# Kernel optimization log

Measured on AMD Instinct MI355X. Metric: run time of the kernel, lower is better.

Reference implementation:

```python
import jax, jax.numpy as jnp
import numpy as np

B, CTX, DRAFT, D = 2, 4096, 512, 2048
H, KVH, HD = 16, 4, 128
N_REP = H // KVH
EPS = 1e-6
THETA = 10000.0
SCALE = 1.0 / np.sqrt(HD).astype(np.float32)


def setup_inputs() -> dict:
    key = jax.random.key(0)
    ks = jax.random.split(key, 6)
    return {
        "draft_hidden": jax.random.normal(ks[0], (B, DRAFT, D), jnp.float32),
        "context_hidden": jax.random.normal(ks[1], (B, CTX, D), jnp.float32),
        "Wq": jax.random.normal(ks[2], (H * HD, D), jnp.float32) * 0.02,
        "Wk": jax.random.normal(ks[3], (KVH * HD, D), jnp.float32) * 0.02,
        "Wv": jax.random.normal(ks[4], (KVH * HD, D), jnp.float32) * 0.02,
        "Wo": jax.random.normal(ks[5], (D, H * HD), jnp.float32) * 0.02,
        "q_norm_w": jnp.ones((HD,), jnp.float32),
        "k_norm_w": jnp.ones((HD,), jnp.float32),
        "context_position_ids": jnp.broadcast_to(jnp.arange(CTX, dtype=jnp.int32), (B, CTX)),
        "draft_position_ids": jnp.broadcast_to(CTX + jnp.arange(DRAFT, dtype=jnp.int32), (B, DRAFT)),
    }


def _rms_norm(x, w):
    # per-head RMSNorm over last dim (head_dim), computed in fp32
    v = jnp.mean(jnp.square(x.astype(jnp.float32)), axis=-1, keepdims=True)
    return (w * (x.astype(jnp.float32) * jax.lax.rsqrt(v + EPS))).astype(x.dtype)


def _rotate_half(x):
    x1, x2 = jnp.split(x, 2, axis=-1)
    return jnp.concatenate((-x2, x1), axis=-1)


def _rope(x, pos):
    # x: [B, nH, S, HD], pos: [B, S] int -> cos/sin gathered per position
    inv_freq = 1.0 / (THETA ** (jnp.arange(0, HD, 2, dtype=jnp.float32) / HD))  # [HD/2]
    freqs = pos.astype(jnp.float32)[:, None, :, None] * inv_freq  # [B,1,S,HD/2]
    emb = jnp.concatenate((freqs, freqs), axis=-1)  # [B,1,S,HD]
    return x * jnp.cos(emb) + _rotate_half(x) * jnp.sin(emb)


def reference(draft_hidden, context_hidden, Wq, Wk, Wv, Wo, q_norm_w, k_norm_w,
              context_position_ids, draft_position_ids):
    bsz, draft_len, _ = draft_hidden.shape
    ctx_len = context_hidden.shape[1]
    total_len = ctx_len + draft_len

    # Q from draft hidden only
    q = (draft_hidden @ Wq.T).reshape(bsz, draft_len, H, HD)
    q = _rms_norm(q, q_norm_w).transpose(0, 2, 1, 3)  # [B,H,Sq,HD]

    # Dual-source KV: context then draft, shared projections
    kv_in = jnp.concatenate([context_hidden, draft_hidden], axis=1)  # [B,total,D]
    k = (kv_in @ Wk.T).reshape(bsz, total_len, KVH, HD)
    v = (kv_in @ Wv.T).reshape(bsz, total_len, KVH, HD).transpose(0, 2, 1, 3)
    k = _rms_norm(k, k_norm_w).transpose(0, 2, 1, 3)  # [B,KVH,total,HD]

    full_position_ids = jnp.concatenate([context_position_ids, draft_position_ids], axis=1)
    q = _rope(q, draft_position_ids)
    k = _rope(k, full_position_ids)

    # GQA expansion (repeat each kv head n_rep times contiguously)
    k = jnp.repeat(k, N_REP, axis=1)  # [B,H,total,HD]
    v = jnp.repeat(v, N_REP, axis=1)

    # full (unmasked) scaled dot-product attention, block_mask=None path
    scores = jnp.einsum('bhqd,bhkd->bhqk', q, k) * SCALE
    probs = jax.nn.softmax(scores, axis=-1)
    attn = jnp.einsum('bhqk,bhkd->bhqd', probs, v)  # [B,H,Sq,HD]

    attn = attn.transpose(0, 2, 1, 3).reshape(bsz, draft_len, H * HD)
    return attn @ Wo.T
```

## Files before the change

### kernel.cpp

```cpp
#include <hip/hip_runtime.h>
#include <stdint.h>

#define B_ 2
#define CTX_ 4096
#define DRAFT_ 512
#define D_ 2048
#define H_ 16
#define KVH_ 4
#define HD_ 128
#define TOT_ 4608
#define NSPLIT 4
#define SPLIT_LEN (TOT_ / NSPLIT)

using bf16x8 = __attribute__((ext_vector_type(8))) short;
using f32x4  = __attribute__((ext_vector_type(4))) float;
using f32x16 = __attribute__((ext_vector_type(16))) float;

__device__ __forceinline__ unsigned short f2bf(float x) {
  unsigned int u = __float_as_uint(x);
  u += 0x7fffu + ((u >> 16) & 1u);
  return (unsigned short)(u >> 16);
}

__device__ __forceinline__ unsigned cvtpk(float lo, float hi) {
  unsigned r;
  asm("v_cvt_pk_bf16_f32 %0, %1, %2" : "=v"(r) : "v"(lo), "v"(hi));
  return r;
}

__device__ __forceinline__ void gload16(const void* g, void* l) {
  __builtin_amdgcn_global_load_lds((const __attribute__((address_space(1))) void*)g,
                                   (__attribute__((address_space(3))) void*)l, 16, 0, 0);
}

__device__ __forceinline__ f32x16 vbroad16(float x) {
  f32x16 v;
#pragma unroll
  for (int i = 0; i < 16; ++i) v[i] = x;
  return v;
}

__global__ __launch_bounds__(256, 4)
void conv_kernel(const float* __restrict__ ctx, const float* __restrict__ draft,
                 const float* __restrict__ wq, const float* __restrict__ wk,
                 const float* __restrict__ wv, const float* __restrict__ wo,
                 unsigned short* __restrict__ kv, unsigned short* __restrict__ wqb,
                 unsigned short* __restrict__ wkb, unsigned short* __restrict__ wvb,
                 unsigned short* __restrict__ wob) {
  long t = (long)blockIdx.x * 256 + threadIdx.x;
  const long NKV = (long)B_ * TOT_ * D_ / 8;
  const long NWQ = 2048L * 2048 / 8;
  const long NWK = 512L * 2048 / 8;
  const float* src;
  unsigned short* dst;
  if (t < NKV) {
    long i = t * 8;
    int b = (int)(i / ((long)TOT_ * D_));
    long rem = i - (long)b * TOT_ * D_;
    int r = (int)(rem / D_);
    int c = (int)(rem - (long)r * D_);
    if (r < CTX_) src = ctx + ((long)(b * CTX_ + r)) * D_ + c;
    else          src = draft + ((long)(b * DRAFT_ + (r - CTX_))) * D_ + c;
    dst = kv + i;
  } else if (t < NKV + NWQ) {
    long l = t - NKV; src = wq + l * 8; dst = wqb + l * 8;
  } else if (t < NKV + NWQ + NWK) {
    long l = t - NKV - NWQ; src = wk + l * 8; dst = wkb + l * 8;
  } else if (t < NKV + NWQ + 2 * NWK) {
    long l = t - NKV - NWQ - NWK; src = wv + l * 8; dst = wvb + l * 8;
  } else {
    long l = t - NKV - NWQ - 2 * NWK; src = wo + l * 8; dst = wob + l * 8;
  }
  float4 a = ((const float4*)src)[0];
  float4 b4 = ((const float4*)src)[1];
  uint4 o;
  o.x = (unsigned)f2bf(a.x) | ((unsigned)f2bf(a.y) << 16);
  o.y = (unsigned)f2bf(a.z) | ((unsigned)f2bf(a.w) << 16);
  o.z = (unsigned)f2bf(b4.x) | ((unsigned)f2bf(b4.y) << 16);
  o.w = (unsigned)f2bf(b4.z) | ((unsigned)f2bf(b4.w) << 16);
  *((uint4*)dst) = o;
}

template <int BM, int BN>
__device__ __forceinline__ void gemm_body(const unsigned short* __restrict__ A,
                                          const unsigned short* __restrict__ W,
                                          float* __restrict__ C, int ld, int kLen,
                                          int N, unsigned short* lds) {
  constexpr int MT = BM / 32;
  constexpr int NT = BN / 32;
  constexpr int BUF = (BM + BN) * 64;
  constexpr int LOADS = BM / 32 + BN / 32;
  const int tid = threadIdx.x;
  const int lane = tid & 63, wid = tid >> 6;
  const int g = lane >> 4, r16 = lane & 15;
  const int wm = wid >> 1, wn = wid & 1;

  f32x4 zero = {0.f, 0.f, 0.f, 0.f};
  f32x4 acc[MT][NT];
#pragma unroll
  for (int i = 0; i < MT; ++i)
#pragma unroll
    for (int j = 0; j < NT; ++j) acc[i][j] = zero;

  auto stage = [&](int kb, unsigned short* buf) {
    unsigned short* As = buf;
    unsigned short* Bs = buf + BM * 64;
#pragma unroll
    for (int is = 0; is < BM / 32; ++is) {
      int row = is * 32 + (tid >> 3);
      int sl = (tid & 7) ^ (row & 7);
      gload16(A + (long)row * ld + kb + sl * 8, As + is * 2048 + wid * 512);
    }
#pragma unroll
    for (int is = 0; is < BN / 32; ++is) {
      int row = is * 32 + (tid >> 3);
      int sl = (tid & 7) ^ (row & 7);
      gload16(W + (long)row * ld + kb + sl * 8, Bs + is * 2048 + wid * 512);
    }
  };

  stage(0, lds);
  const int nk = kLen >> 6;
  for (int t = 0; t < nk; ++t) {
    if (t + 1 < nk) {
      stage((t + 1) << 6, lds + ((t + 1) & 1) * BUF);
      if constexpr (LOADS == 8)      asm volatile("s_waitcnt vmcnt(8)" ::: "memory");
      else if constexpr (LOADS == 6) asm volatile("s_waitcnt vmcnt(6)" ::: "memory");
      else if constexpr (LOADS == 4) asm volatile("s_waitcnt vmcnt(4)" ::: "memory");
      else                           asm volatile("s_waitcnt vmcnt(0)" ::: "memory");
    } else {
      asm volatile("s_waitcnt vmcnt(0)" ::: "memory");
    }
    __builtin_amdgcn_s_barrier();
    __builtin_amdgcn_sched_barrier(0);
    unsigned short* As = lds + (t & 1) * BUF;
    unsigned short* Bs = As + BM * 64;
#pragma unroll
    for (int kh = 0; kh < 2; ++kh) {
      bf16x8 af[MT], bfr[NT];
#pragma unroll
      for (int i = 0; i < MT; ++i) {
        int row = wm * (BM / 2) + i * 16 + r16;
        int sl = (kh * 4 + g) ^ (row & 7);
        af[i] = *(const bf16x8*)(As + row * 64 + sl * 8);
      }
#pragma unroll
      for (int j = 0; j < NT; ++j) {
        int row = wn * (BN / 2) + j * 16 + r16;
        int sl = (kh * 4 + g) ^ (row & 7);
        bfr[j] = *(const bf16x8*)(Bs + row * 64 + sl * 8);
      }
#pragma unroll
      for (int i = 0; i < MT; ++i)
#pragma unroll
        for (int j = 0; j < NT; ++j)
          acc[i][j] = __builtin_amdgcn_mfma_f32_16x16x32_bf16(af[i], bfr[j], acc[i][j], 0, 0, 0);
    }
    __builtin_amdgcn_sched_barrier(0);
    __builtin_amdgcn_s_barrier();
  }
#pragma unroll
  for (int i = 0; i < MT; ++i)
#pragma unroll
    for (int j = 0; j < NT; ++j)
#pragma unroll
      for (int e = 0; e < 4; ++e) {
        int row = wm * (BM / 2) + i * 16 + g * 4 + e;
        int col = wn * (BN / 2) + j * 16 + r16;
        C[(long)row * N + col] = acc[i][j][e];
      }
}

__global__ __launch_bounds__(256, 2)
void qkv_kernel(const unsigned short* __restrict__ kvb,
                const unsigned short* __restrict__ wqb,
                const unsigned short* __restrict__ wkvb, float* __restrict__ qraw,
                float* __restrict__ kvraw) {
  __shared__ unsigned short lds[2 * 256 * 64];
  int id = (blockIdx.x & 7) * 88 + (blockIdx.x >> 3);
  if (id < 128) {
    int b = id >> 6, mb = (id >> 4) & 3, nb = id & 15;
    const unsigned short* A = kvb + ((long)b * TOT_ + CTX_ + mb * 128) * 2048;
    const unsigned short* W = wqb + (long)nb * 128 * 2048;
    float* C = qraw + ((long)b * 512 + mb * 128) * 2048 + nb * 128;
    gemm_body<128, 128>(A, W, C, 2048, 2048, 2048, lds);
  } else {
    int id2 = id - 128;
    int mb = id2 >> 3, nb = id2 & 7;
    const unsigned short* A = kvb + (long)mb * 128 * 2048;
    const unsigned short* W = wkvb + (long)nb * 128 * 2048;
    float* C = kvraw + (long)mb * 128 * 1024 + nb * 128;
    gemm_body<128, 128>(A, W, C, 2048, 2048, 1024, lds);
  }
}

__global__ __launch_bounds__(256, 3)
void ogemm_kernel(const unsigned short* __restrict__ attb,
                  const unsigned short* __restrict__ wob, float* __restrict__ out) {
  __shared__ unsigned short lds[2 * 128 * 64];
  int sw = (blockIdx.x & 7) * 64 + (blockIdx.x >> 3);
  int nb = sw >> 4, mb = sw & 15;
  const unsigned short* A = attb + (long)mb * 64 * 2048;
  const unsigned short* W = wob + (long)nb * 64 * 2048;
  float* C = out + (long)mb * 64 * 2048 + nb * 64;
  gemm_body<64, 64>(A, W, C, 2048, 2048, 2048, lds);
}

__global__ __launch_bounds__(256, 4)
void post_kernel(const float* __restrict__ qraw, const float* __restrict__ kvraw,
                 const float* __restrict__ qw, const float* __restrict__ kw,
                 const int* __restrict__ cpos, const int* __restrict__ dpos,
                 unsigned short* __restrict__ qatt, unsigned short* __restrict__ katt,
                 unsigned short* __restrict__ vt) {
  const int QB = (B_ * DRAFT_ * H_) / 4;
  const int KB = (B_ * TOT_ * KVH_) / 4;
  int bid = blockIdx.x;
  int tid = threadIdx.x;
  int lane = tid & 63, wid = tid >> 6;
  if (bid < QB + KB) {
    bool isQ = (bid < QB);
    int row = (isQ ? bid : bid - QB) * 4 + wid;
    const float* src;
    const float* wnorm;
    int pos;
    float fold;
    unsigned short* dst;
    if (isQ) {
      int b = row >> 13;
      int r2 = row & 8191;
      int s = r2 >> 4, hh = r2 & 15;
      src = qraw + (long)row * 128;
      wnorm = qw;
      pos = dpos[b * DRAFT_ + s];
      fold = 0.08838834764831843f * 1.4426950408889634f;
      dst = qatt + ((long)(b * H_ + hh) * DRAFT_ + s) * 128;
    } else {
      int b = row / (TOT_ * KVH_);
      int r2 = row - b * (TOT_ * KVH_);
      int s = r2 >> 2, hh = r2 & 3;
      src = kvraw + ((long)(b * TOT_ + s)) * 1024 + hh * 128;
      wnorm = kw;
      pos = (s < CTX_) ? cpos[b * CTX_ + s] : dpos[b * DRAFT_ + (s - CTX_)];
      fold = 1.0f;
      dst = katt + ((long)(b * KVH_ + hh) * TOT_ + s) * 128;
    }
    float x1 = src[lane], x2 = src[lane + 64];
    float ss = x1 * x1 + x2 * x2;
#pragma unroll
    for (int off = 1; off < 64; off <<= 1) ss += __shfl_xor(ss, off);
    float rn = rsqrtf(ss * 0.0078125f + 1e-6f);
    float y1 = wnorm[lane] * x1 * rn;
    float y2 = wnorm[lane + 64] * x2 * rn;
    float invf = exp2f((float)lane * -0.20762050593046014f);
    float fr = (float)pos * invf;
    float sn, cs;
    sincosf(fr, &sn, &cs);
    dst[lane] = f2bf((y1 * cs - y2 * sn) * fold);
    dst[lane + 64] = f2bf((y2 * cs + y1 * sn) * fold);
  } else {
    long t = (long)(bid - (QB + KB)) * 256 + tid;
    int d = (int)(t & 127);
    int rest = (int)(t >> 7);
    int sc = rest % 576, bk = rest / 576;
    int b = bk >> 2, kvh = bk & 3;
    int s0 = sc * 8;
    const float* src = kvraw + ((long)(b * TOT_ + s0)) * 1024 + 512 + kvh * 128 + d;
    unsigned int o[4];
#pragma unroll
    for (int jj = 0; jj < 4; ++jj) {
      unsigned short lo = f2bf(src[(2 * jj) * 1024]);
      unsigned short hi = f2bf(src[(2 * jj + 1) * 1024]);
      o[jj] = (unsigned)lo | ((unsigned)hi << 16);
    }
    int k0 = s0 & 63;
    long dstbase = ((long)(bk * 128 + d)) * TOT_ + (s0 & ~63) + (k0 & 48) + ((k0 & 8) >> 1);
    *(uint2*)(vt + dstbase) = make_uint2(o[0], o[1]);
    *(uint2*)(vt + dstbase + 8) = make_uint2(o[2], o[3]);
  }
}

__global__ __launch_bounds__(512, 2)
void attn_kernel(const unsigned short* __restrict__ Q, const unsigned short* __restrict__ Kt,
                 const unsigned short* __restrict__ Vt, float* __restrict__ pO,
                 float* __restrict__ pL) {
  __shared__ unsigned short lds[2 * 16384];
  const int tid = threadIdx.x, lane = tid & 63, wid = tid >> 6;
  const int hi = lane >> 5, l31 = lane & 31;
  int sw = ((blockIdx.x & 7) << 5) | (blockIdx.x >> 3);
  const int q0 = sw & 1, h = (sw >> 1) & 15, z = sw >> 5;
  const int b = z >> 2, split = z & 3;
  const int kvh = h >> 2;
  const float M = 16.4f;

  const unsigned short* Qb =
      Q + ((long)(b * H_ + h) * DRAFT_ + q0 * 256 + wid * 32) * 128;
  bf16x8 qf[8];
#pragma unroll
  for (int ks = 0; ks < 8; ++ks)
    qf[ks] = *(const bf16x8*)(Qb + l31 * 128 + ks * 16 + hi * 8);

  f32x16 acc[4];
#pragma unroll
  for (int nb = 0; nb < 4; ++nb) acc[nb] = vbroad16(0.f);
  float l_run = 0.0f;

  const unsigned short* Kbase = Kt + (long)(b * KVH_ + kvh) * TOT_ * 128;
  const unsigned short* Vbase = Vt + (long)(b * KVH_ + kvh) * 128L * TOT_;

  auto stage = [&](int s0, int c) {
    unsigned short* Ks = lds + c * 16384;
    unsigned short* Vs = Ks + 8192;
#pragma unroll
    for (int is = 0; is < 2; ++is) {
      int row = is * 32 + (tid >> 4);
      int sl = (tid & 15) ^ (row & 7);
      gload16(Kbase + (long)(s0 + row) * 128 + sl * 8, Ks + is * 4096 + wid * 512);
    }
#pragma unroll
    for (int is = 0; is < 2; ++is) {
      int d = is * 64 + (tid >> 3);
      int sl = (tid & 7) ^ (d & 7);
      gload16(Vbase + (long)d * TOT_ + s0 + sl * 8, Vs + is * 4096 + wid * 512);
    }
  };

  const int sBeg = split * SPLIT_LEN;
  const int NTile = SPLIT_LEN / 64;
  stage(sBeg, 0);
  int cur = 0;
  for (int t = 0; t < NTile; ++t) {
    if (t + 1 < NTile) {
      stage(sBeg + (t + 1) * 64, cur ^ 1);
      asm volatile("s_waitcnt vmcnt(4)" ::: "memory");
    } else {
      asm volatile("s_waitcnt vmcnt(0)" ::: "memory");
    }
    __builtin_amdgcn_s_barrier();
    __builtin_amdgcn_sched_barrier(0);
    const char* KsB = (const char*)(lds + cur * 16384);
    const char* VsB = KsB + 16384;

    f32x16 st0 = vbroad16(-M), st1 = vbroad16(-M);
    __builtin_amdgcn_s_setprio(1);
#pragma unroll
    for (int ks = 0; ks < 8; ++ks) {
      int gsl = ks * 2 + hi;
      bf16x8 a0 = *(const bf16x8*)(KsB + l31 * 256 + ((gsl ^ (l31 & 7)) * 16));
      bf16x8 a1 = *(const bf16x8*)(KsB + (32 + l31) * 256 + ((gsl ^ (l31 & 7)) * 16));
      st0 = __builtin_amdgcn_mfma_f32_32x32x16_bf16(a0, qf[ks], st0, 0, 0, 0);
      st1 = __builtin_amdgcn_mfma_f32_32x32x16_bf16(a1, qf[ks], st1, 0, 0, 0);
    }
    __builtin_amdgcn_s_setprio(0);

    float l_own = 0.0f;
    unsigned pkA[8];
#pragma unroll
    for (int m = 0; m < 8; ++m) {
      float e0 = exp2f(st0[2 * m]), e1 = exp2f(st0[2 * m + 1]);
      l_own += e0 + e1;
      pkA[m] = cvtpk(e0, e1);
    }
    union { unsigned u[4]; bf16x8 v; } pf01[2], pf23[2];
#pragma unroll
    for (int m = 0; m < 4; ++m) {
      pf01[0].u[m] = pkA[m];
      pf01[1].u[m] = pkA[m + 4];
    }
    __builtin_amdgcn_s_setprio(1);
#pragma unroll
    for (int nb = 0; nb < 4; ++nb) {
      int d = nb * 32 + l31;
#pragma unroll
      for (int k2 = 0; k2 < 2; ++k2) {
        bf16x8 a = *(const bf16x8*)(VsB + d * 128 + (((k2 * 2 + hi) ^ (d & 7)) * 16));
        acc[nb] = __builtin_amdgcn_mfma_f32_32x32x16_bf16(a, pf01[k2].v, acc[nb], 0, 0, 0);
      }
    }
    __builtin_amdgcn_sched_barrier(0);
    unsigned pkB[8];
#pragma unroll
    for (int m = 0; m < 8; ++m) {
      float e0 = exp2f(st1[2 * m]), e1 = exp2f(st1[2 * m + 1]);
      l_own += e0 + e1;
      pkB[m] = cvtpk(e0, e1);
    }
#pragma unroll
    for (int m = 0; m < 4; ++m) {
      pf23[0].u[m] = pkB[m];
      pf23[1].u[m] = pkB[m + 4];
    }
    l_run += l_own;
#pragma unroll
    for (int nb = 0; nb < 4; ++nb) {
      int d = nb * 32 + l31;
#pragma unroll
      for (int k2 = 0; k2 < 2; ++k2) {
        bf16x8 a = *(const bf16x8*)(VsB + d * 128 + ((((k2 + 2) * 2 + hi) ^ (d & 7)) * 16));
        acc[nb] = __builtin_amdgcn_mfma_f32_32x32x16_bf16(a, pf23[k2].v, acc[nb], 0, 0, 0);
      }
    }
    __builtin_amdgcn_s_setprio(0);
    __builtin_amdgcn_sched_barrier(0);
    __builtin_amdgcn_s_barrier();
    cur ^= 1;
  }
  l_run += __shfl_xor(l_run, 32);

  const long R = (long)B_ * H_ * DRAFT_;
  const int q = q0 * 256 + wid * 32 + l31;
  const long rowIdx = ((long)(b * H_ + h)) * DRAFT_ + q;
  const long pbase = ((long)split * R + rowIdx) * 128;
#pragma unroll
  for (int nb = 0; nb < 4; ++nb)
#pragma unroll
    for (int r4 = 0; r4 < 4; ++r4) {
      int d0 = nb * 32 + 8 * r4 + 4 * hi;
      float4 v = make_float4(acc[nb][4 * r4 + 0], acc[nb][4 * r4 + 1],
                             acc[nb][4 * r4 + 2], acc[nb][4 * r4 + 3]);
      *(float4*)(pO + pbase + d0) = v;
    }
  if (hi == 0) pL[(long)split * R + rowIdx] = l_run;
}

__global__ __launch_bounds__(256, 4)
void acomb_kernel(const float* __restrict__ pO, const float* __restrict__ pL,
                  unsigned short* __restrict__ attb) {
  const long R = (long)B_ * H_ * DRAFT_;
  int row = blockIdx.x * 2 + (threadIdx.x >> 7);
  int d = threadIdx.x & 127;
  float ltot = 0.0f, o = 0.0f;
#pragma unroll
  for (int i = 0; i < NSPLIT; ++i) {
    ltot += pL[(long)i * R + row];
    o += pO[((long)i * R + row) * 128 + d];
  }
  o /= ltot;
  int bh = row >> 9, q = row & 511;
  int b = bh >> 4, h = bh & 15;
  attb[(((long)(b * 512 + q) * 16 + h)) * 128 + d] = f2bf(o);
}

extern "C" void kernel_launch(void* const* d_in, const int* in_sizes, int n_in,
                              void* d_out, int out_size, void* d_ws, size_t ws_size,
                              hipStream_t stream) {
  const float* draft = (const float*)d_in[0];
  const float* ctx = (const float*)d_in[1];
  const float* Wq = (const float*)d_in[2];
  const float* Wk = (const float*)d_in[3];
  const float* Wv = (const float*)d_in[4];
  const float* Wo = (const float*)d_in[5];
  const float* qw = (const float*)d_in[6];
  const float* kw = (const float*)d_in[7];
  const int* cpos = (const int*)d_in[8];
  const int* dpos = (const int*)d_in[9];

  char* ws = (char*)d_ws;
  unsigned short* kvb = (unsigned short*)(ws + 0);
  unsigned short* wqb = (unsigned short*)(ws + 37748736);
  unsigned short* wkb = (unsigned short*)(ws + 46137344);
  unsigned short* wvb = (unsigned short*)(ws + 48234496);
  unsigned short* wob = (unsigned short*)(ws + 50331648);
  float* qraw = (float*)(ws + 58720256);
  float* kvraw = (float*)(ws + 67108864);
  float* pO = (float*)(ws + 67108864);
  float* pL = (float*)(ws + 100663296);
  unsigned short* qatt = (unsigned short*)(ws + 104857600);
  unsigned short* katt = (unsigned short*)(ws + 109051904);
  unsigned short* vtb = (unsigned short*)(ws + 118489088);
  unsigned short* attb = (unsigned short*)(ws + 127926272);

  conv_kernel<<<dim3(14336), 256, 0, stream>>>(ctx, draft, Wq, Wk, Wv, Wo, kvb, wqb,
                                               wkb, wvb, wob);
  qkv_kernel<<<dim3(704), 256, 0, stream>>>(kvb, wqb, wkb, qraw, kvraw);
  post_kernel<<<dim3(15616), 256, 0, stream>>>(qraw, kvraw, qw, kw, cpos, dpos, qatt,
                                               katt, vtb);
  attn_kernel<<<dim3(256), 512, 0, stream>>>(qatt, katt, vtb, pO, pL);
  acomb_kernel<<<dim3(8192), 256, 0, stream>>>(pO, pL, attb);
  ogemm_kernel<<<dim3(512), 256, 0, stream>>>(attb, wob, (float*)d_out);
}
```

Before: 174.2 us.

## Fuse RMSNorm, RoPE and V transpose into QKV GEMM epilogue via LDS

The QKV projection GEMM now stages its fp32 output tile in shared memory and applies the per-head RMSNorm, RoPE, scaling and bf16 conversion (or the V transpose/pack) directly in the epilogue. This removes the separate post_kernel launch and the round trip of the fp32 qraw/kvraw intermediates through global memory. The epilogue runs on fewer, larger blocks, so its sincos and shuffle work is serialized per block and may lengthen the GEMM kernel's tail.

```diff
diff --git a/kernel.cpp b/kernel.cpp
--- a/kernel.cpp
+++ b/kernel.cpp
@@ -81,7 +81,7 @@
   *((uint4*)dst) = o;
 }
 
-template <int BM, int BN>
+template <int BM, int BN, bool TO_LDS = false>
 __device__ __forceinline__ void gemm_body(const unsigned short* __restrict__ A,
                                           const unsigned short* __restrict__ W,
                                           float* __restrict__ C, int ld, int kLen,
@@ -159,38 +159,120 @@
     __builtin_amdgcn_sched_barrier(0);
     __builtin_amdgcn_s_barrier();
   }
-#pragma unroll
-  for (int i = 0; i < MT; ++i)
-#pragma unroll
-    for (int j = 0; j < NT; ++j)
-#pragma unroll
-      for (int e = 0; e < 4; ++e) {
-        int row = wm * (BM / 2) + i * 16 + g * 4 + e;
-        int col = wn * (BN / 2) + j * 16 + r16;
-        C[(long)row * N + col] = acc[i][j][e];
-      }
+  if constexpr (TO_LDS) {
+    float* F = (float*)lds;
+#pragma unroll
+    for (int i = 0; i < MT; ++i)
+#pragma unroll
+      for (int j = 0; j < NT; ++j)
+#pragma unroll
+        for (int e = 0; e < 4; ++e)
+          F[(wm * 64 + i * 16 + g * 4 + e) * 128 + wn * 64 + j * 16 + r16] = acc[i][j][e];
+  } else {
+#pragma unroll
+    for (int i = 0; i < MT; ++i)
+#pragma unroll
+      for (int j = 0; j < NT; ++j)
+#pragma unroll
+        for (int e = 0; e < 4; ++e) {
+          int row = wm * (BM / 2) + i * 16 + g * 4 + e;
+          int col = wn * (BN / 2) + j * 16 + r16;
+          C[(long)row * N + col] = acc[i][j][e];
+        }
+  }
 }
 
 __global__ __launch_bounds__(256, 2)
 void qkv_kernel(const unsigned short* __restrict__ kvb,
                 const unsigned short* __restrict__ wqb,
-                const unsigned short* __restrict__ wkvb, float* __restrict__ qraw,
-                float* __restrict__ kvraw) {
+                const unsigned short* __restrict__ wkvb,
+                const float* __restrict__ qw, const float* __restrict__ kw,
+                const int* __restrict__ cpos, const int* __restrict__ dpos,
+                unsigned short* __restrict__ qatt, unsigned short* __restrict__ katt,
+                unsigned short* __restrict__ vt) {
   __shared__ unsigned short lds[2 * 256 * 64];
+  float* F = (float*)lds;
+  const int tid = threadIdx.x;
+  const int lane = tid & 63, wid = tid >> 6;
   int id = (blockIdx.x & 7) * 88 + (blockIdx.x >> 3);
+
   if (id < 128) {
-    int b = id >> 6, mb = (id >> 4) & 3, nb = id & 15;
+    int b = id >> 6, mb = (id >> 4) & 3, hh = id & 15;
     const unsigned short* A = kvb + ((long)b * TOT_ + CTX_ + mb * 128) * 2048;
-    const unsigned short* W = wqb + (long)nb * 128 * 2048;
-    float* C = qraw + ((long)b * 512 + mb * 128) * 2048 + nb * 128;
-    gemm_body<128, 128>(A, W, C, 2048, 2048, 2048, lds);
+    const unsigned short* W = wqb + (long)hh * 128 * 2048;
+    gemm_body<128, 128, true>(A, W, nullptr, 2048, 2048, 0, lds);
+    __syncthreads();
+    const float fold = 0.08838834764831843f * 1.4426950408889634f;
+    float invf = exp2f((float)lane * -0.20762050593046014f);
+    float w1 = qw[lane], w2 = qw[lane + 64];
+#pragma unroll 4
+    for (int rr = 0; rr < 32; ++rr) {
+      int r = wid * 32 + rr;
+      int s = mb * 128 + r;
+      float x1 = F[r * 128 + lane], x2 = F[r * 128 + lane + 64];
+      float ss = x1 * x1 + x2 * x2;
+#pragma unroll
+      for (int off = 1; off < 64; off <<= 1) ss += __shfl_xor(ss, off);
+      float rn = rsqrtf(ss * 0.0078125f + 1e-6f);
+      float y1 = w1 * x1 * rn, y2 = w2 * x2 * rn;
+      int pos = dpos[b * DRAFT_ + s];
+      float fr = (float)pos * invf, sn, cs;
+      sincosf(fr, &sn, &cs);
+      unsigned short* dst = qatt + ((long)(b * H_ + hh) * DRAFT_ + s) * 128;
+      dst[lane] = f2bf((y1 * cs - y2 * sn) * fold);
+      dst[lane + 64] = f2bf((y2 * cs + y1 * sn) * fold);
+    }
   } else {
     int id2 = id - 128;
     int mb = id2 >> 3, nb = id2 & 7;
     const unsigned short* A = kvb + (long)mb * 128 * 2048;
     const unsigned short* W = wkvb + (long)nb * 128 * 2048;
-    float* C = kvraw + (long)mb * 128 * 1024 + nb * 128;
-    gemm_body<128, 128>(A, W, C, 2048, 2048, 1024, lds);
+    gemm_body<128, 128, true>(A, W, nullptr, 2048, 2048, 0, lds);
+    __syncthreads();
+    int bb = mb / 36;
+    int sbase = (mb % 36) * 128;
+    if (nb < 4) {
+      int kvh = nb;
+      float invf = exp2f((float)lane * -0.20762050593046014f);
+      float w1 = kw[lane], w2 = kw[lane + 64];
+#pragma unroll 4
+      for (int rr = 0; rr < 32; ++rr) {
+        int r = wid * 32 + rr;
+        int s = sbase + r;
+        float x1 = F[r * 128 + lane], x2 = F[r * 128 + lane + 64];
+        float ss = x1 * x1 + x2 * x2;
+#pragma unroll
+        for (int off = 1; off < 64; off <<= 1) ss += __shfl_xor(ss, off);
+        float rn = rsqrtf(ss * 0.0078125f + 1e-6f);
+        float y1 = w1 * x1 * rn, y2 = w2 * x2 * rn;
+        int pos = (s < CTX_) ? cpos[bb * CTX_ + s] : dpos[bb * DRAFT_ + (s - CTX_)];
+        float fr = (float)pos * invf, sn, cs;
+        sincosf(fr, &sn, &cs);
+        unsigned short* dst = katt + ((long)(bb * KVH_ + kvh) * TOT_ + s) * 128;
+        dst[lane] = f2bf(y1 * cs - y2 * sn);
+        dst[lane + 64] = f2bf(y2 * cs + y1 * sn);
+      }
+    } else {
+      int kvh = nb - 4;
+      int d = tid & 127;
+      int g0 = tid >> 7;
+      unsigned short* vrow = vt + ((long)((bb * KVH_ + kvh) * 128 + d)) * TOT_;
+#pragma unroll
+      for (int gi = 0; gi < 8; ++gi) {
+        int s0 = (g0 + 2 * gi) * 8;
+        unsigned o[4];
+#pragma unroll
+        for (int jj = 0; jj < 4; ++jj) {
+          unsigned short lo = f2bf(F[(s0 + 2 * jj) * 128 + d]);
+          unsigned short hi = f2bf(F[(s0 + 2 * jj + 1) * 128 + d]);
+          o[jj] = (unsigned)lo | ((unsigned)hi << 16);
+        }
+        int k0 = s0 & 63;
+        long dstbase = sbase + (s0 & ~63) + (k0 & 48) + ((k0 & 8) >> 1);
+        *(uint2*)(vrow + dstbase) = make_uint2(o[0], o[1]);
+        *(uint2*)(vrow + dstbase + 8) = make_uint2(o[2], o[3]);
+      }
+    }
   }
 }
 
@@ -204,79 +286,6 @@
   const unsigned short* W = wob + (long)nb * 64 * 2048;
   float* C = out + (long)mb * 64 * 2048 + nb * 64;
   gemm_body<64, 64>(A, W, C, 2048, 2048, 2048, lds);
-}
-
-__global__ __launch_bounds__(256, 4)
-void post_kernel(const float* __restrict__ qraw, const float* __restrict__ kvraw,
-                 const float* __restrict__ qw, const float* __restrict__ kw,
-                 const int* __restrict__ cpos, const int* __restrict__ dpos,
-                 unsigned short* __restrict__ qatt, unsigned short* __restrict__ katt,
-                 unsigned short* __restrict__ vt) {
-  const int QB = (B_ * DRAFT_ * H_) / 4;
-  const int KB = (B_ * TOT_ * KVH_) / 4;
-  int bid = blockIdx.x;
-  int tid = threadIdx.x;
-  int lane = tid & 63, wid = tid >> 6;
-  if (bid < QB + KB) {
-    bool isQ = (bid < QB);
-    int row = (isQ ? bid : bid - QB) * 4 + wid;
-    const float* src;
-    const float* wnorm;
-    int pos;
-    float fold;
-    unsigned short* dst;
-    if (isQ) {
-      int b = row >> 13;
-      int r2 = row & 8191;
-      int s = r2 >> 4, hh = r2 & 15;
-      src = qraw + (long)row * 128;
-      wnorm = qw;
-      pos = dpos[b * DRAFT_ + s];
-      fold = 0.08838834764831843f * 1.4426950408889634f;
-      dst = qatt + ((long)(b * H_ + hh) * DRAFT_ + s) * 128;
-    } else {
-      int b = row / (TOT_ * KVH_);
-      int r2 = row - b * (TOT_ * KVH_);
-      int s = r2 >> 2, hh = r2 & 3;
-      src = kvraw + ((long)(b * TOT_ + s)) * 1024 + hh * 128;
-      wnorm = kw;
-      pos = (s < CTX_) ? cpos[b * CTX_ + s] : dpos[b * DRAFT_ + (s - CTX_)];
-      fold = 1.0f;
-      dst = katt + ((long)(b * KVH_ + hh) * TOT_ + s) * 128;
-    }
-    float x1 = src[lane], x2 = src[lane + 64];
-    float ss = x1 * x1 + x2 * x2;
-#pragma unroll
-    for (int off = 1; off < 64; off <<= 1) ss += __shfl_xor(ss, off);
-    float rn = rsqrtf(ss * 0.0078125f + 1e-6f);
-    float y1 = wnorm[lane] * x1 * rn;
-    float y2 = wnorm[lane + 64] * x2 * rn;
-    float invf = exp2f((float)lane * -0.20762050593046014f);
-    float fr = (float)pos * invf;
-    float sn, cs;
-    sincosf(fr, &sn, &cs);
-    dst[lane] = f2bf((y1 * cs - y2 * sn) * fold);
-    dst[lane + 64] = f2bf((y2 * cs + y1 * sn) * fold);
-  } else {
-    long t = (long)(bid - (QB + KB)) * 256 + tid;
-    int d = (int)(t & 127);
-    int rest = (int)(t >> 7);
-    int sc = rest % 576, bk = rest / 576;
-    int b = bk >> 2, kvh = bk & 3;
-    int s0 = sc * 8;
-    const float* src = kvraw + ((long)(b * TOT_ + s0)) * 1024 + 512 + kvh * 128 + d;
-    unsigned int o[4];
-#pragma unroll
-    for (int jj = 0; jj < 4; ++jj) {
-      unsigned short lo = f2bf(src[(2 * jj) * 1024]);
-      unsigned short hi = f2bf(src[(2 * jj + 1) * 1024]);
-      o[jj] = (unsigned)lo | ((unsigned)hi << 16);
-    }
-    int k0 = s0 & 63;
-    long dstbase = ((long)(bk * 128 + d)) * TOT_ + (s0 & ~63) + (k0 & 48) + ((k0 & 8) >> 1);
-    *(uint2*)(vt + dstbase) = make_uint2(o[0], o[1]);
-    *(uint2*)(vt + dstbase + 8) = make_uint2(o[2], o[3]);
-  }
 }
 
 __global__ __launch_bounds__(512, 2)
@@ -460,8 +469,6 @@
   unsigned short* wkb = (unsigned short*)(ws + 46137344);
   unsigned short* wvb = (unsigned short*)(ws + 48234496);
   unsigned short* wob = (unsigned short*)(ws + 50331648);
-  float* qraw = (float*)(ws + 58720256);
-  float* kvraw = (float*)(ws + 67108864);
   float* pO = (float*)(ws + 67108864);
   float* pL = (float*)(ws + 100663296);
   unsigned short* qatt = (unsigned short*)(ws + 104857600);
@@ -471,9 +478,8 @@
 
   conv_kernel<<<dim3(14336), 256, 0, stream>>>(ctx, draft, Wq, Wk, Wv, Wo, kvb, wqb,
                                                wkb, wvb, wob);
-  qkv_kernel<<<dim3(704), 256, 0, stream>>>(kvb, wqb, wkb, qraw, kvraw);
-  post_kernel<<<dim3(15616), 256, 0, stream>>>(qraw, kvraw, qw, kw, cpos, dpos, qatt,
-                                               katt, vtb);
+  qkv_kernel<<<dim3(704), 256, 0, stream>>>(kvb, wqb, wkb, qw, kw, cpos, dpos, qatt,
+                                            katt, vtb);
   attn_kernel<<<dim3(256), 512, 0, stream>>>(qatt, katt, vtb, pO, pL);
   acomb_kernel<<<dim3(8192), 256, 0, stream>>>(pO, pL, attb);
   ogemm_kernel<<<dim3(512), 256, 0, stream>>>(attb, wob, (float*)d_out);
```

Result: slower. 178.1 us (+2.3%).
